# Optimization experiments

Hardware: AMD Instinct MI355X
Metric: run time of the kernel (lower is better)

Reference implementation:

```python
import jax, jax.numpy as jnp
import numpy as np


def setup_inputs() -> dict:
    key = jax.random.key(0)
    ks = jax.random.split(key, 9)
    B, T, S, D = 4, 256, 256, 512
    scale = 1.0 / np.sqrt(D)
    inp = {
        "output": jax.random.normal(ks[0], (B, T, D), dtype=jnp.float32),
        "context": jax.random.normal(ks[1], (B, S, D), dtype=jnp.float32),
        "mask": jax.random.randint(ks[2], (B, S), 0, 2, dtype=jnp.int32),
        # learned params (nn.Linear stores y = x @ W.T + b; we store W.T directly)
        "Wq": jax.random.normal(ks[3], (D, D), dtype=jnp.float32) * scale,
        "bq": jax.random.normal(ks[4], (D,), dtype=jnp.float32) * scale,
        "Wc": jax.random.normal(ks[5], (D, D), dtype=jnp.float32) * scale,
        "v": jax.random.normal(ks[6], (D,), dtype=jnp.float32) * scale,
        "Wout": jax.random.normal(ks[7], (2 * D, D), dtype=jnp.float32) * scale,
        "bout": jax.random.normal(ks[8], (D,), dtype=jnp.float32) * scale,
    }
    return inp


def reference(output, context, mask, Wq, bq, Wc, v, Wout, bout):
    # output: (B, T, D) decoder states; context: (B, S, D) encoder states
    wq = jnp.einsum("btd,de->bte", output, Wq) + bq          # (B, T, D)
    uh = jnp.einsum("bsd,de->bse", context, Wc)               # (B, S, D)
    # additive score: v . tanh(wq + uh), broadcast over (T, S)
    wquh = jnp.tanh(wq[:, :, None, :] + uh[:, None, :, :])    # (B, T, S, D)
    score = jnp.einsum("btsd,d->bts", wquh, v)                # (B, T, S)
    # masked softmax exactly as the torch code: max over ALL positions,
    # then zero out masked entries (mask==1 means masked) and renormalize.
    max_by_row = jnp.max(score, axis=-1, keepdims=True)
    keep = (1.0 - mask.astype(score.dtype))[:, None, :]       # (B, 1, S)
    attn = jnp.exp(score - max_by_row) * keep
    attn = attn / jnp.sum(attn, axis=-1, keepdims=True)       # (B, T, S)
    mix = jnp.einsum("bts,bsd->btd", attn, context)           # (B, T, D)
    combined = jnp.concatenate([mix, output], axis=-1)        # (B, T, 2D)
    out = jnp.einsum("btf,fd->btd", combined, Wout) + bout    # (B, T, D)
    return out, attn
```

## Files before the change

kernel.cpp:

```cpp
#include <hip/hip_runtime.h>
#include <hip/hip_bf16.h>

#define B_ 4
#define T_ 256
#define S_ 256
#define D_ 512
#define TB 2

typedef __bf16 bf16x8 __attribute__((ext_vector_type(8)));
typedef float  floatx4 __attribute__((ext_vector_type(4)));

#define C2F 2.885390081777926f

static __device__ __forceinline__ unsigned short f2bf(float x) {
    __hip_bfloat16 h = __float2bfloat16(x);
    return *reinterpret_cast<unsigned short*>(&h);
}
static __device__ __forceinline__ float asf(unsigned int u) {
    float f; __builtin_memcpy(&f, &u, 4); return f;
}


__global__ __launch_bounds__(256) void prep(
    const float* __restrict__ output, const float* __restrict__ context,
    const float* __restrict__ Wq, const float* __restrict__ Wc,
    const float* __restrict__ Wout,
    unsigned short* __restrict__ out_f, unsigned short* __restrict__ ctx_f,
    unsigned short* __restrict__ Wq_f, unsigned short* __restrict__ Wc_f,
    unsigned short* __restrict__ WoT_f, unsigned short* __restrict__ WoB_f)
{
    const int tid = threadIdx.x;
    const int z = blockIdx.z;

    if (z >= 4) {
        const float* src = (z == 4) ? output : context;
        unsigned short* dst = (z == 4) ? out_f : ctx_f;
        const int bid  = blockIdx.y * 16 + blockIdx.x;
        const int tile = bid * 4 + (tid >> 6);
        const int lane = tid & 63;
        const int mblk = tile >> 4, kblk = tile & 15;
        const float* s = src + (size_t)(mblk * 16 + (lane & 15)) * 512
                             + kblk * 32 + (lane >> 4) * 8;
        float4 a = *(const float4*)s;
        float4 b = *(const float4*)(s + 4);
        uint4 pk;
        pk.x = (unsigned)f2bf(a.x) | ((unsigned)f2bf(a.y) << 16);
        pk.y = (unsigned)f2bf(a.z) | ((unsigned)f2bf(a.w) << 16);
        pk.z = (unsigned)f2bf(b.x) | ((unsigned)f2bf(b.y) << 16);
        pk.w = (unsigned)f2bf(b.z) | ((unsigned)f2bf(b.w) << 16);
        *(uint4*)(dst + (size_t)tile * 512 + lane * 8) = pk;
        return;
    }

    const float* W; unsigned short* WF; int krow0;
    if      (z == 0) { W = Wq;   WF = Wq_f;  krow0 = 0;   }
    else if (z == 1) { W = Wc;   WF = Wc_f;  krow0 = 0;   }
    else if (z == 2) { W = Wout; WF = WoT_f; krow0 = 0;   }
    else             { W = Wout; WF = WoB_f; krow0 = 512; }

    const int n0 = blockIdx.x * 32;
    const int k0 = blockIdx.y * 32;

    __shared__ float tile[32][33];
    const int c = tid & 31, r = tid >> 5;
    #pragma unroll
    for (int i = 0; i < 4; ++i)
        tile[r + 8 * i][c] = W[(size_t)(krow0 + k0 + r + 8 * i) * 512 + n0 + c];
    __syncthreads();
    #pragma unroll
    for (int i = 0; i < 4; ++i) {
        const int n = n0 + r + 8 * i;
        const int k = k0 + c;
        const int tl = (n >> 4) * 16 + (k >> 5);
        const int ln = (n & 15) | (((k >> 3) & 3) << 4);
        WF[((size_t)tl * 64 + ln) * 8 + (k & 7)] = f2bf(tile[c][r + 8 * i]);
    }
}

struct GArgs {
    const unsigned short* Af;
    const unsigned short* Bf;
    const float* aux;
    void* C;
    int mode;
};

__global__ __launch_bounds__(256) void gemm2(GArgs g0, GArgs g1, GArgs g2, GArgs g3)
{
    const int z = blockIdx.z;
    GArgs g = (z == 0) ? g0 : (z == 1) ? g1 : (z == 2) ? g2 : g3;

    const int tid  = threadIdx.x;
    const int wave = tid >> 6, lane = tid & 63;
    const int l15  = lane & 15, quad = lane >> 4;
    const int mblk = blockIdx.y * 4 + wave;
    const int nb0  = blockIdx.x * 2;

    const unsigned short* Ap  = g.Af + ((size_t)mblk * 16 * 64 + lane) * 8;
    const unsigned short* Bp0 = g.Bf + ((size_t)nb0 * 16 * 64 + lane) * 8;
    const unsigned short* Bp1 = Bp0 + (size_t)16 * 64 * 8;

    floatx4 acc[2];
    acc[0] = (floatx4){0.f, 0.f, 0.f, 0.f};
    acc[1] = (floatx4){0.f, 0.f, 0.f, 0.f};

    #pragma unroll 4
    for (int k = 0; k < 16; ++k) {
        bf16x8 a  = *(const bf16x8*)(Ap  + k * 512);
        bf16x8 b0 = *(const bf16x8*)(Bp0 + k * 512);
        bf16x8 b1 = *(const bf16x8*)(Bp1 + k * 512);
        acc[0] = __builtin_amdgcn_mfma_f32_16x16x32_bf16(a, b0, acc[0], 0, 0, 0);
        acc[1] = __builtin_amdgcn_mfma_f32_16x16x32_bf16(a, b1, acc[1], 0, 0, 0);
    }

    #pragma unroll
    for (int ni = 0; ni < 2; ++ni) {
        const int col = (nb0 + ni) * 16 + l15;
        const int rbase = mblk * 16 + quad * 4;
        if (g.mode == 3) {
            unsigned short* Cb = (unsigned short*)g.C;
            #pragma unroll
            for (int r = 0; r < 4; ++r) {
                int row = rbase + r, bb = row >> 8, ss = row & 255;
                Cb[((size_t)(bb * 64 + (col >> 3)) * 256 + ss) * 8 + (col & 7)]
                    = f2bf(C2F * acc[ni][r]);
            }
        } else if (g.mode == 5) {
            unsigned short* Cb = (unsigned short*)g.C;
            #pragma unroll
            for (int r = 0; r < 4; ++r)
                Cb[(size_t)(rbase + r) * 512 + col] = f2bf(acc[ni][r]);
        } else {
            float* Cf = (float*)g.C;
            float bv = g.aux ? g.aux[col] : 0.0f;
            #pragma unroll
            for (int r = 0; r < 4; ++r) {
                float val = acc[ni][r] + bv;
                if (g.mode == 1) val *= C2F;
                Cf[(size_t)(rbase + r) * 512 + col] = val;
            }
        }
    }
}

__global__ __launch_bounds__(1024) void attn_fused(
    const float* __restrict__ wqs,
    const unsigned short* __restrict__ uhb,
    const unsigned short* __restrict__ CWb,
    const float* __restrict__ OB,
    const int*   __restrict__ mask,
    const float* __restrict__ v,
    float* __restrict__ attn_out,
    float* __restrict__ out)
{
    const int bg  = blockIdx.x;
    const int b   = bg / (T_ / TB);
    const int t0  = (bg % (T_ / TB)) * TB;
    const int tid = threadIdx.x;
    const int s   = tid & 255;
    const int h   = tid >> 8;

    __shared__ float  w_s[TB][D_];
    __shared__ float  v_s[D_];
    __shared__ float2 part[4][256];
    __shared__ float2 wred[4];
    __shared__ float  a_s[TB][256];
    __shared__ float  mixp[4][TB][D_];

    if (tid < 512) {
        w_s[0][tid] = wqs[(size_t)(b * T_ + t0 + 0) * D_ + tid];
        w_s[1][tid] = wqs[(size_t)(b * T_ + t0 + 1) * D_ + tid];
        v_s[tid]    = v[tid];
    }
    __syncthreads();

    float acc0 = 0.f, acc1 = 0.f;
    const int dd0 = h * 16;
    const uint4* u4 = (const uint4*)(uhb + ((size_t)(b * 64 + dd0) * 256 + s) * 8);

    #pragma unroll 4
    for (int dd = 0; dd < 16; ++dd) {
        uint4 uu = u4[(size_t)dd * 256];
        float uf[8];
        uf[0] = asf(uu.x << 16); uf[1] = asf(uu.x & 0xffff0000u);
        uf[2] = asf(uu.y << 16); uf[3] = asf(uu.y & 0xffff0000u);
        uf[4] = asf(uu.z << 16); uf[5] = asf(uu.z & 0xffff0000u);
        uf[6] = asf(uu.w << 16); uf[7] = asf(uu.w & 0xffff0000u);

        const int dbase = (dd0 + dd) * 8;
        #pragma unroll
        for (int j = 0; j < 8; ++j) {
            float vv = v_s[dbase + j];
            float x0 = w_s[0][dbase + j] + uf[j];
            float x1 = w_s[1][dbase + j] + uf[j];
            float r0 = __builtin_amdgcn_rcpf(__builtin_amdgcn_exp2f(x0) + 1.0f);
            float r1 = __builtin_amdgcn_rcpf(__builtin_amdgcn_exp2f(x1) + 1.0f);
            acc0 = fmaf(vv, r0, acc0);
            acc1 = fmaf(vv, r1, acc1);
        }
    }
    part[h][s] = make_float2(acc0, acc1);
    __syncthreads();

    float p0 = 0.f, p1 = 0.f;
    if (tid < 256) {
        float A0 = part[0][tid].x + part[1][tid].x + part[2][tid].x + part[3][tid].x;
        float A1 = part[0][tid].y + part[1][tid].y + part[2][tid].y + part[3][tid].y;
        float keep = 1.0f - (float)mask[b * S_ + tid];
        p0 = __builtin_amdgcn_exp2f(-C2F * A0) * keep;
        p1 = __builtin_amdgcn_exp2f(-C2F * A1) * keep;
        float s0 = p0, s1 = p1;
        #pragma unroll
        for (int off = 1; off < 64; off <<= 1) {
            s0 += __shfl_xor(s0, off);
            s1 += __shfl_xor(s1, off);
        }
        if ((tid & 63) == 0) wred[tid >> 6] = make_float2(s0, s1);
    }
    __syncthreads();

    if (tid < 256) {
        float den0 = wred[0].x + wred[1].x + wred[2].x + wred[3].x;
        float den1 = wred[0].y + wred[1].y + wred[2].y + wred[3].y;
        float a0 = p0 * __builtin_amdgcn_rcpf(den0);
        float a1 = p1 * __builtin_amdgcn_rcpf(den1);
        attn_out[(size_t)(b * T_ + t0 + 0) * S_ + tid] = a0;
        attn_out[(size_t)(b * T_ + t0 + 1) * S_ + tid] = a1;
        a_s[0][tid] = a0;
        a_s[1][tid] = a1;
    }
    __syncthreads();

    const int d2 = tid & 255;
    const int sh = h * 64;
    const unsigned short* cw = CWb + ((size_t)(b * S_) + sh) * D_ + 2 * d2;
    float m[TB][2] = {};
    #pragma unroll 8
    for (int s2 = 0; s2 < 64; ++s2) {
        unsigned int cc = *(const unsigned int*)(cw + (size_t)s2 * D_);
        float c0 = asf(cc << 16), c1 = asf(cc & 0xffff0000u);
        #pragma unroll
        for (int t = 0; t < TB; ++t) {
            float a = a_s[t][sh + s2];
            m[t][0] = fmaf(a, c0, m[t][0]);
            m[t][1] = fmaf(a, c1, m[t][1]);
        }
    }
    #pragma unroll
    for (int t = 0; t < TB; ++t) {
        mixp[h][t][2 * d2]     = m[t][0];
        mixp[h][t][2 * d2 + 1] = m[t][1];
    }
    __syncthreads();

    {
        const int t = tid >> 9, d = tid & 511;
        size_t idx = (size_t)(b * T_ + t0 + t) * D_ + d;
        out[idx] = mixp[0][t][d] + mixp[1][t][d] + mixp[2][t][d] + mixp[3][t][d]
                 + OB[idx];
    }
}

extern "C" void kernel_launch(void* const* d_in, const int* in_sizes, int n_in,
                              void* d_out, int out_size, void* d_ws, size_t ws_size,
                              hipStream_t stream) {
    const float* output  = (const float*)d_in[0];
    const float* context = (const float*)d_in[1];
    const int*   mask    = (const int*)d_in[2];
    const float* Wq      = (const float*)d_in[3];
    const float* bq      = (const float*)d_in[4];
    const float* Wc      = (const float*)d_in[5];
    const float* v       = (const float*)d_in[6];
    const float* Wout    = (const float*)d_in[7];
    const float* bout    = (const float*)d_in[8];

    float* out  = (float*)d_out;
    float* attn = out + (size_t)B_ * T_ * D_;

    char* ws = (char*)d_ws;
    float* wqs           = (float*)ws;
    float* OB            = (float*)(ws + (2u << 20));
    unsigned short* uhb   = (unsigned short*)(ws + (4u << 20));
    unsigned short* out_f = (unsigned short*)(ws + (5u << 20));
    unsigned short* ctx_f = (unsigned short*)(ws + (6u << 20));
    unsigned short* Wq_f  = (unsigned short*)(ws + (7u << 20));
    unsigned short* Wc_f  = (unsigned short*)(ws + (7u << 20) + (512u << 10));
    unsigned short* WoT_f = (unsigned short*)(ws + (8u << 20));
    unsigned short* WoB_f = (unsigned short*)(ws + (8u << 20) + (512u << 10));
    unsigned short* CWb   = (unsigned short*)(ws + (9u << 20));

    dim3 blk(256);

    prep<<<dim3(16, 16, 6), blk, 0, stream>>>(
        output, context, Wq, Wc, Wout, out_f, ctx_f, Wq_f, Wc_f, WoT_f, WoB_f);

    GArgs gwq = { out_f, Wq_f,  bq,      wqs, 1 };
    GArgs guh = { ctx_f, Wc_f,  nullptr, uhb, 3 };
    GArgs gob = { out_f, WoB_f, bout,    OB,  4 };
    GArgs gcw = { ctx_f, WoT_f, nullptr, CWb, 5 };
    gemm2<<<dim3(16, 16, 4), blk, 0, stream>>>(gwq, guh, gob, gcw);

    attn_fused<<<dim3(B_ * T_ / TB), dim3(1024), 0, stream>>>(
        wqs, uhb, CWb, OB, mask, v, attn, out);
}
```

Before: 122.3 us.

## Precompute exponentials in GEMM epilogues and pair reciprocals in tanh-score loop

The additive-attention inner loop used to evaluate exp2 and a reciprocal per (t,s,d) element. Now the wq and uh GEMM epilogues store exp(2wq) and exp(-2uh) directly, and the score loop computes sigmoid-like terms as G/(H+G), combining two terms over one reciprocal. This cuts transcendental work in the O(B·T·S·D) loop. In exchange the uh buffer is stored as fp32 instead of bf16, doubling its load traffic, and clamping the exponentials risks precision or overflow issues for large inputs.

```diff
diff --git a/kernel.cpp b/kernel.cpp
--- a/kernel.cpp
+++ b/kernel.cpp
@@ -18,6 +18,9 @@
 }
 static __device__ __forceinline__ float asf(unsigned int u) {
     float f; __builtin_memcpy(&f, &u, 4); return f;
+}
+static __device__ __forceinline__ float clamp_pos(float x) {
+    return fminf(fmaxf(x, 1e-15f), 1e15f);
 }
 
 
@@ -117,13 +120,22 @@
     for (int ni = 0; ni < 2; ++ni) {
         const int col = (nb0 + ni) * 16 + l15;
         const int rbase = mblk * 16 + quad * 4;
-        if (g.mode == 3) {
-            unsigned short* Cb = (unsigned short*)g.C;
+        if (g.mode == 1) {
+            float* Cf = (float*)g.C;
+            float bv = g.aux[col];
+            #pragma unroll
+            for (int r = 0; r < 4; ++r) {
+                float hh = __builtin_amdgcn_exp2f(C2F * (acc[ni][r] + bv));
+                Cf[(size_t)(rbase + r) * 512 + col] = clamp_pos(hh);
+            }
+        } else if (g.mode == 3) {
+            float* Cf = (float*)g.C;
             #pragma unroll
             for (int r = 0; r < 4; ++r) {
                 int row = rbase + r, bb = row >> 8, ss = row & 255;
-                Cb[((size_t)(bb * 64 + (col >> 3)) * 256 + ss) * 8 + (col & 7)]
-                    = f2bf(C2F * acc[ni][r]);
+                float gg = __builtin_amdgcn_exp2f(-C2F * acc[ni][r]);
+                Cf[((size_t)(bb * 128 + (col >> 2)) * 256 + ss) * 4 + (col & 3)]
+                    = clamp_pos(gg);
             }
         } else if (g.mode == 5) {
             unsigned short* Cb = (unsigned short*)g.C;
@@ -132,20 +144,17 @@
                 Cb[(size_t)(rbase + r) * 512 + col] = f2bf(acc[ni][r]);
         } else {
             float* Cf = (float*)g.C;
-            float bv = g.aux ? g.aux[col] : 0.0f;
+            float bv = g.aux[col];
             #pragma unroll
-            for (int r = 0; r < 4; ++r) {
-                float val = acc[ni][r] + bv;
-                if (g.mode == 1) val *= C2F;
-                Cf[(size_t)(rbase + r) * 512 + col] = val;
-            }
+            for (int r = 0; r < 4; ++r)
+                Cf[(size_t)(rbase + r) * 512 + col] = acc[ni][r] + bv;
         }
     }
 }
 
 __global__ __launch_bounds__(1024) void attn_fused(
-    const float* __restrict__ wqs,
-    const unsigned short* __restrict__ uhb,
+    const float* __restrict__ Hb,
+    const float* __restrict__ Gb,
     const unsigned short* __restrict__ CWb,
     const float* __restrict__ OB,
     const int*   __restrict__ mask,
@@ -168,35 +177,40 @@
     __shared__ float  mixp[4][TB][D_];
 
     if (tid < 512) {
-        w_s[0][tid] = wqs[(size_t)(b * T_ + t0 + 0) * D_ + tid];
-        w_s[1][tid] = wqs[(size_t)(b * T_ + t0 + 1) * D_ + tid];
+        w_s[0][tid] = Hb[(size_t)(b * T_ + t0 + 0) * D_ + tid];
+        w_s[1][tid] = Hb[(size_t)(b * T_ + t0 + 1) * D_ + tid];
         v_s[tid]    = v[tid];
     }
     __syncthreads();
 
     float acc0 = 0.f, acc1 = 0.f;
-    const int dd0 = h * 16;
-    const uint4* u4 = (const uint4*)(uhb + ((size_t)(b * 64 + dd0) * 256 + s) * 8);
+    const float* gbase = Gb + ((size_t)(b * 128 + h * 32) * 256 + s) * 4;
 
     #pragma unroll 4
     for (int dd = 0; dd < 16; ++dd) {
-        uint4 uu = u4[(size_t)dd * 256];
-        float uf[8];
-        uf[0] = asf(uu.x << 16); uf[1] = asf(uu.x & 0xffff0000u);
-        uf[2] = asf(uu.y << 16); uf[3] = asf(uu.y & 0xffff0000u);
-        uf[4] = asf(uu.z << 16); uf[5] = asf(uu.z & 0xffff0000u);
-        uf[6] = asf(uu.w << 16); uf[7] = asf(uu.w & 0xffff0000u);
-
-        const int dbase = (dd0 + dd) * 8;
+        float4 ga = *(const float4*)(gbase + dd * 2048);
+        float4 gb = *(const float4*)(gbase + dd * 2048 + 1024);
+        const int dbase = (h * 16 + dd) * 8;
+        float4 va  = *(const float4*)&v_s[dbase];
+        float4 vb  = *(const float4*)&v_s[dbase + 4];
+        float4 h0a = *(const float4*)&w_s[0][dbase];
+        float4 h0b = *(const float4*)&w_s[0][dbase + 4];
+        float4 h1a = *(const float4*)&w_s[1][dbase];
+        float4 h1b = *(const float4*)&w_s[1][dbase + 4];
+        float G[8]  = {ga.x,  ga.y,  ga.z,  ga.w,  gb.x,  gb.y,  gb.z,  gb.w};
+        float V[8]  = {va.x,  va.y,  va.z,  va.w,  vb.x,  vb.y,  vb.z,  vb.w};
+        float H0[8] = {h0a.x, h0a.y, h0a.z, h0a.w, h0b.x, h0b.y, h0b.z, h0b.w};
+        float H1[8] = {h1a.x, h1a.y, h1a.z, h1a.w, h1b.x, h1b.y, h1b.z, h1b.w};
         #pragma unroll
-        for (int j = 0; j < 8; ++j) {
-            float vv = v_s[dbase + j];
-            float x0 = w_s[0][dbase + j] + uf[j];
-            float x1 = w_s[1][dbase + j] + uf[j];
-            float r0 = __builtin_amdgcn_rcpf(__builtin_amdgcn_exp2f(x0) + 1.0f);
-            float r1 = __builtin_amdgcn_rcpf(__builtin_amdgcn_exp2f(x1) + 1.0f);
-            acc0 = fmaf(vv, r0, acc0);
-            acc1 = fmaf(vv, r1, acc1);
+        for (int p = 0; p < 4; ++p) {
+            float G0 = G[2 * p], G1 = G[2 * p + 1];
+            float P0 = V[2 * p] * G0, P1 = V[2 * p + 1] * G1;
+            float D00 = G0 + H0[2 * p], D01 = G1 + H0[2 * p + 1];
+            acc0 = fmaf(fmaf(P0, D01, P1 * D00),
+                        __builtin_amdgcn_rcpf(D00 * D01), acc0);
+            float D10 = G0 + H1[2 * p], D11 = G1 + H1[2 * p + 1];
+            acc1 = fmaf(fmaf(P0, D11, P1 * D10),
+                        __builtin_amdgcn_rcpf(D10 * D11), acc1);
         }
     }
     part[h][s] = make_float2(acc0, acc1);
@@ -278,28 +292,28 @@
     float* attn = out + (size_t)B_ * T_ * D_;
 
     char* ws = (char*)d_ws;
-    float* wqs           = (float*)ws;
-    float* OB            = (float*)(ws + (2u << 20));
-    unsigned short* uhb   = (unsigned short*)(ws + (4u << 20));
-    unsigned short* out_f = (unsigned short*)(ws + (5u << 20));
-    unsigned short* ctx_f = (unsigned short*)(ws + (6u << 20));
-    unsigned short* Wq_f  = (unsigned short*)(ws + (7u << 20));
-    unsigned short* Wc_f  = (unsigned short*)(ws + (7u << 20) + (512u << 10));
-    unsigned short* WoT_f = (unsigned short*)(ws + (8u << 20));
-    unsigned short* WoB_f = (unsigned short*)(ws + (8u << 20) + (512u << 10));
-    unsigned short* CWb   = (unsigned short*)(ws + (9u << 20));
+    float* Hb             = (float*)ws;
+    float* OB             = (float*)(ws + (2u << 20));
+    float* Gb             = (float*)(ws + (4u << 20));
+    unsigned short* out_f = (unsigned short*)(ws + (6u << 20));
+    unsigned short* ctx_f = (unsigned short*)(ws + (7u << 20));
+    unsigned short* Wq_f  = (unsigned short*)(ws + (8u << 20));
+    unsigned short* Wc_f  = (unsigned short*)(ws + (8u << 20) + (512u << 10));
+    unsigned short* WoT_f = (unsigned short*)(ws + (9u << 20));
+    unsigned short* WoB_f = (unsigned short*)(ws + (9u << 20) + (512u << 10));
+    unsigned short* CWb   = (unsigned short*)(ws + (10u << 20));
 
     dim3 blk(256);
 
     prep<<<dim3(16, 16, 6), blk, 0, stream>>>(
         output, context, Wq, Wc, Wout, out_f, ctx_f, Wq_f, Wc_f, WoT_f, WoB_f);
 
-    GArgs gwq = { out_f, Wq_f,  bq,      wqs, 1 };
-    GArgs guh = { ctx_f, Wc_f,  nullptr, uhb, 3 };
+    GArgs gwq = { out_f, Wq_f,  bq,      Hb,  1 };
+    GArgs guh = { ctx_f, Wc_f,  nullptr, Gb,  3 };
     GArgs gob = { out_f, WoB_f, bout,    OB,  4 };
     GArgs gcw = { ctx_f, WoT_f, nullptr, CWb, 5 };
     gemm2<<<dim3(16, 16, 4), blk, 0, stream>>>(gwq, guh, gob, gcw);
 
     attn_fused<<<dim3(B_ * T_ / TB), dim3(1024), 0, stream>>>(
-        wqs, uhb, CWb, OB, mask, v, attn, out);
-}
+        Hb, Gb, CWb, OB, mask, v, attn, out);
+}
```

After: 119.8 us. 2.1% less time.
